# Optimization experiments

Hardware: AMD Instinct MI355X
Metric: run time of the kernel (lower is better)

The kernel has to match this reference:

```python
import jax, jax.numpy as jnp
import numpy as np

TEMPERATURE = 0.1
N, D = 8192, 1024

def setup_inputs() -> dict:
    key = jax.random.key(0)
    k1, k2 = jax.random.split(key)
    im = jax.random.normal(k1, (N, D), dtype=jnp.float32)
    cap = jax.random.normal(k2, (N, D), dtype=jnp.float32)
    return {"im": im, "cap": cap}

def reference(im, cap):
    # InfoNCE (info_nce package) L2-normalizes query, positive and negatives.
    # Per-sample loop: for image i, positive = cap[i], negatives = cap[j != i].
    # Logits set = sim(im_i, cap_j) for all j, positive at j == i, so
    # loss_i = logsumexp_j(S[i, j] / T) - S[i, i] / T  (CLIP-style CE).
    imn = im / jnp.linalg.norm(im, axis=-1, keepdims=True)
    capn = cap / jnp.linalg.norm(cap, axis=-1, keepdims=True)
    S = jnp.einsum('id,jd->ij', imn, capn) / TEMPERATURE  # [N, N]
    diag = jnp.diagonal(S)
    loss_i2c = jax.nn.logsumexp(S, axis=1) - diag  # image -> caption direction
    loss_c2i = jax.nn.logsumexp(S, axis=0) - diag  # caption -> image direction
    # original averages all 2N per-sample losses
    return 0.5 * (jnp.mean(loss_i2c) + jnp.mean(loss_c2i))
```

## Files before the change

kernel.cpp:

```cpp
#include <hip/hip_runtime.h>
#include <stdint.h>

#define N_ 8192
#define D_ 1024
#define EPILOGUE_SCALE (10.0f / 256.0f)
#define ENC_SCALE 16.0f
#define SLAB 262144

typedef float f32x4 __attribute__((ext_vector_type(4)));

#define GLD16(gsrc, ldst)                                                    \
  __builtin_amdgcn_global_load_lds(                                          \
      (const __attribute__((address_space(1))) unsigned int*)(gsrc),         \
      (__attribute__((address_space(3))) unsigned int*)(ldst), 16, 0, 0)


__global__ __launch_bounds__(1024) void normalize_k(
    const float* __restrict__ im, const float* __restrict__ cap,
    unsigned int* __restrict__ imn, unsigned int* __restrict__ capn,
    float* __restrict__ diag, float* __restrict__ sums ) {
  __shared__ unsigned int ldsA[16 * 257];
  __shared__ unsigned int ldsB[16 * 257];
  const int til = blockIdx.x;
  const int t = threadIdx.x;
  if (til < 4) ((float4*)sums)[til * 1024 + t] = (float4){0.f, 0.f, 0.f, 0.f};

  const int r = t >> 6, j = t & 63;
  const int row = til * 16 + r;
  const float4* __restrict__ aR = (const float4*)(im + (size_t)row * D_);
  const float4* __restrict__ bR = (const float4*)(cap + (size_t)row * D_);

  float4 a0 = aR[j], a1 = aR[j + 64], a2 = aR[j + 128], a3 = aR[j + 192];
  float4 b0 = bR[j], b1 = bR[j + 64], b2 = bR[j + 128], b3 = bR[j + 192];

  float ssa = a0.x * a0.x + a0.y * a0.y + a0.z * a0.z + a0.w * a0.w
            + a1.x * a1.x + a1.y * a1.y + a1.z * a1.z + a1.w * a1.w
            + a2.x * a2.x + a2.y * a2.y + a2.z * a2.z + a2.w * a2.w
            + a3.x * a3.x + a3.y * a3.y + a3.z * a3.z + a3.w * a3.w;
  float ssb = b0.x * b0.x + b0.y * b0.y + b0.z * b0.z + b0.w * b0.w
            + b1.x * b1.x + b1.y * b1.y + b1.z * b1.z + b1.w * b1.w
            + b2.x * b2.x + b2.y * b2.y + b2.z * b2.z + b2.w * b2.w
            + b3.x * b3.x + b3.y * b3.y + b3.z * b3.z + b3.w * b3.w;
  float dt  = a0.x * b0.x + a0.y * b0.y + a0.z * b0.z + a0.w * b0.w
            + a1.x * b1.x + a1.y * b1.y + a1.z * b1.z + a1.w * b1.w
            + a2.x * b2.x + a2.y * b2.y + a2.z * b2.z + a2.w * b2.w
            + a3.x * b3.x + a3.y * b3.y + a3.z * b3.z + a3.w * b3.w;
#pragma unroll
  for (int o = 1; o < 64; o <<= 1) {
    ssa += __shfl_xor(ssa, o, 64);
    ssb += __shfl_xor(ssb, o, 64);
    dt  += __shfl_xor(dt, o, 64);
  }
  const float ra = rsqrtf(ssa), rb = rsqrtf(ssb);
  if (j == 0) diag[row] = dt * ra * rb * 10.0f;
  const float sa = ra * ENC_SCALE, sb = rb * ENC_SCALE;

#define CVT_ST(av, bv, ofs)                                                  \
  {                                                                          \
    int pa_ = __builtin_amdgcn_cvt_pk_fp8_f32(av.x * sa, av.y * sa, 0, false); \
    pa_ = __builtin_amdgcn_cvt_pk_fp8_f32(av.z * sa, av.w * sa, pa_, true);  \
    int pb_ = __builtin_amdgcn_cvt_pk_fp8_f32(bv.x * sb, bv.y * sb, 0, false); \
    pb_ = __builtin_amdgcn_cvt_pk_fp8_f32(bv.z * sb, bv.w * sb, pb_, true);  \
    ldsA[r * 257 + j + (ofs)] = (unsigned int)pa_;                           \
    ldsB[r * 257 + j + (ofs)] = (unsigned int)pb_;                           \
  }
  CVT_ST(a0, b0, 0)
  CVT_ST(a1, b1, 64)
  CVT_ST(a2, b2, 128)
  CVT_ST(a3, b3, 192)
#undef CVT_ST
  __syncthreads();

  {
    const int s = t >> 5, c4 = t & 31;
    const int fl0 = c4 * 2, fl1 = fl0 + 1;
    const int i0 = (fl0 & 15) * 257 + s * 8 + (fl0 >> 4) * 2;
    const int i1 = (fl1 & 15) * 257 + s * 8 + (fl1 >> 4) * 2;
    uint4 va, vb;
    va.x = ldsA[i0]; va.y = ldsA[i0 + 1];
    va.z = ldsA[i1]; va.w = ldsA[i1 + 1];
    vb.x = ldsB[i0]; vb.y = ldsB[i0 + 1];
    vb.z = ldsB[i1]; vb.w = ldsB[i1 + 1];
    const size_t d = (size_t)s * 65536 + (size_t)til * 128 + c4 * 4;
    *(uint4*)(imn + d) = va;
    *(uint4*)(capn + d) = vb;
  }
}

__global__ __launch_bounds__(512, 2) void gemm_lse_k(
    const unsigned char* __restrict__ A,
    const unsigned char* __restrict__ B,
    float* __restrict__ rowsum, float* __restrict__ colsum) {
  __shared__ unsigned char lds[4][32768];
  const int t = threadIdx.x;
  const int w = t >> 6, l = t & 63;

  const int bid = blockIdx.x + (blockIdx.y << 5);
  const int nid = (bid & 7) * 128 + (bid >> 3);
  const int rowT = ((nid >> 7) << 2) + (nid & 3);
  const int colT = (nid & 127) >> 2;

  const size_t baseA = (size_t)rowT * 8192;
  const size_t baseB = (size_t)colT * 8192;

  const unsigned char* __restrict__ P = (w < 4) ? A : B;
  const size_t pbase = (w < 4) ? baseA : baseB;
  const int wo = (w & 3) * 4096;
  const int lhalf = (w < 4) ? 0 : 16384;

#define STAGE(kt, cb)                                                        \
  {                                                                          \
    const unsigned char* ps = P + (size_t)(kt) * (2 * (size_t)SLAB) + pbase; \
    _Pragma("unroll")                                                        \
    for (int c = 0; c < 4; ++c) {                                            \
      const int o = wo + c * 1024;                                           \
      GLD16(ps + (size_t)(o >> 13) * SLAB + (o & 8191) + l * 16,             \
            &lds[cb][lhalf + o]);                                            \
    }                                                                        \
  }

  const int wr = w >> 2, wc = w & 3;
  const int aoff = wr * 8 * 512 + l * 8;
  const int boff = 16384 + wc * 4 * 512 + l * 8;

  f32x4 acc[8][4];
#pragma unroll
  for (int m = 0; m < 8; ++m)
#pragma unroll
    for (int n = 0; n < 4; ++n) acc[m][n] = (f32x4){0.f, 0.f, 0.f, 0.f};

#define COMPUTE(cb)                                                          \
  {                                                                          \
    const unsigned char* Lc = &lds[cb][0];                                   \
    _Pragma("unroll")                                                        \
    for (int si = 0; si < 2; ++si) {                                         \
      long a_[8], b_[4];                                                     \
      _Pragma("unroll")                                                      \
      for (int m = 0; m < 8; ++m)                                            \
        a_[m] = *(const long*)(Lc + si * 8192 + aoff + m * 512);             \
      _Pragma("unroll")                                                      \
      for (int n = 0; n < 4; ++n)                                            \
        b_[n] = *(const long*)(Lc + si * 8192 + boff + n * 512);             \
      _Pragma("unroll")                                                      \
      for (int m = 0; m < 8; ++m)                                            \
        _Pragma("unroll")                                                    \
        for (int n = 0; n < 4; ++n)                                          \
          acc[m][n] = __builtin_amdgcn_mfma_f32_16x16x32_fp8_fp8(            \
              a_[m], b_[n], acc[m][n], 0, 0, 0);                             \
    }                                                                        \
  }

  STAGE(0, 0)
  STAGE(1, 1)
  STAGE(2, 2)

#pragma unroll 1
  for (int kt = 0; kt < 13; ++kt) {
    STAGE(kt + 3, (kt + 3) & 3)
    asm volatile("s_waitcnt vmcnt(12)" ::: "memory");
    __builtin_amdgcn_s_barrier();
    COMPUTE(kt & 3)
    __builtin_amdgcn_s_barrier();
  }
  asm volatile("s_waitcnt vmcnt(8)" ::: "memory");
  __builtin_amdgcn_s_barrier();
  COMPUTE(1)
  __builtin_amdgcn_s_barrier();
  asm volatile("s_waitcnt vmcnt(4)" ::: "memory");
  __builtin_amdgcn_s_barrier();
  COMPUTE(2)
  __builtin_amdgcn_s_barrier();
  asm volatile("s_waitcnt vmcnt(0)" ::: "memory");
  __builtin_amdgcn_s_barrier();
  COMPUTE(3)
#undef COMPUTE
#undef STAGE

#pragma unroll
  for (int m = 0; m < 8; ++m)
#pragma unroll
    for (int n = 0; n < 4; ++n)
#pragma unroll
      for (int r = 0; r < 4; ++r)
        acc[m][n][r] = __expf(acc[m][n][r] * EPILOGUE_SCALE);

  const int rowBase = rowT * 256 + wr * 128;
  const int colBase = colT * 256 + wc * 64;
#pragma unroll
  for (int m = 0; m < 8; ++m)
#pragma unroll
    for (int r = 0; r < 4; ++r) {
      float v = 0.f;
#pragma unroll
      for (int n = 0; n < 4; ++n) v += acc[m][n][r];
      v += __shfl_xor(v, 1, 64);
      v += __shfl_xor(v, 2, 64);
      v += __shfl_xor(v, 4, 64);
      v += __shfl_xor(v, 8, 64);
      if ((l & 15) == 0)
        atomicAdd(&rowsum[rowBase + m * 16 + (l >> 4) * 4 + r], v);
    }
#pragma unroll
  for (int n = 0; n < 4; ++n) {
    float v = 0.f;
#pragma unroll
    for (int m = 0; m < 8; ++m)
      v += acc[m][n][0] + acc[m][n][1] + acc[m][n][2] + acc[m][n][3];
    v += __shfl_xor(v, 16, 64);
    v += __shfl_xor(v, 32, 64);
    if (l < 16)
      atomicAdd(&colsum[colBase + n * 16 + l], v);
  }
}

__global__ __launch_bounds__(256) void finalize_k(
    const float* __restrict__ rowsum, const float* __restrict__ colsum,
    const float* __restrict__ diag, float* __restrict__ out) {
  const int t = threadIdx.x;
  float lse = 0.f, dg = 0.f;
  for (int i = t; i < N_; i += 256) {
    lse += __logf(rowsum[i]) + __logf(colsum[i]);
    dg += diag[i];
  }
#pragma unroll
  for (int o = 32; o > 0; o >>= 1) {
    lse += __shfl_down(lse, o, 64);
    dg  += __shfl_down(dg, o, 64);
  }
  __shared__ float red[2][4];
  const int w = t >> 6, l = t & 63;
  if (l == 0) { red[0][w] = lse; red[1][w] = dg; }
  __syncthreads();
  if (t == 0) {
    lse = red[0][0] + red[0][1] + red[0][2] + red[0][3];
    dg  = red[1][0] + red[1][1] + red[1][2] + red[1][3];
    out[0] = 0.5f * lse / (float)N_ - dg / (float)N_;
  }
}

extern "C" void kernel_launch(void* const* d_in, const int* in_sizes, int n_in,
                              void* d_out, int out_size, void* d_ws, size_t ws_size,
                              hipStream_t stream) {
  const float* im = (const float*)d_in[0];
  const float* cap = (const float*)d_in[1];
  float* out = (float*)d_out;
  char* ws = (char*)d_ws;
  unsigned char* imn = (unsigned char*)ws;
  unsigned char* capn = imn + (size_t)N_ * D_;
  float* rowsum = (float*)(ws + 2 * (size_t)N_ * D_);
  float* colsum = rowsum + N_;
  float* diag = colsum + N_;

  normalize_k<<<512, 1024, 0, stream>>>(im, cap, (unsigned int*)imn,
                                        (unsigned int*)capn, diag, rowsum);
  gemm_lse_k<<<dim3(32, 32), 512, 0, stream>>>(imn, capn, rowsum, colsum);
  finalize_k<<<1, 256, 0, stream>>>(rowsum, colsum, diag, out);
}
```

Baseline: 214.7 us.

## Split each k-tile into two phases interleaving LDS reads, global loads and MFMAs

Restructures the FP8 GEMM main loop so each k-tile is processed in two sub-phases. Each phase reads its LDS fragments, issues half of the next tile's global-to-LDS loads, then runs the MFMA block under raised wave priority with a sched_barrier. The aim is finer-grained overlap of memory traffic with matrix math and less contention between waves. The cost is twice as many workgroup barriers per tile, and the hand-placed vmcnt waits must match the new load ordering.

```diff
diff --git a/kernel.cpp b/kernel.cpp
--- a/kernel.cpp
+++ b/kernel.cpp
@@ -108,15 +108,13 @@
   const int wo = (w & 3) * 4096;
   const int lhalf = (w < 4) ? 0 : 16384;
 
-#define STAGE(kt, cb)                                                        \
+#define STAGE2(ps, sb, c0)                                                   \
   {                                                                          \
-    const unsigned char* ps = P + (size_t)(kt) * (2 * (size_t)SLAB) + pbase; \
-    _Pragma("unroll")                                                        \
-    for (int c = 0; c < 4; ++c) {                                            \
-      const int o = wo + c * 1024;                                           \
-      GLD16(ps + (size_t)(o >> 13) * SLAB + (o & 8191) + l * 16,             \
-            &lds[cb][lhalf + o]);                                            \
-    }                                                                        \
+    const int oA_ = wo + (c0) * 1024, oB_ = oA_ + 1024;                      \
+    GLD16((ps) + (size_t)(oA_ >> 13) * SLAB + (oA_ & 8191) + l * 16,         \
+          &lds[sb][lhalf + oA_]);                                            \
+    GLD16((ps) + (size_t)(oB_ >> 13) * SLAB + (oB_ & 8191) + l * 16,         \
+          &lds[sb][lhalf + oB_]);                                            \
   }
 
   const int wr = w >> 2, wc = w & 3;
@@ -129,52 +127,72 @@
 #pragma unroll
     for (int n = 0; n < 4; ++n) acc[m][n] = (f32x4){0.f, 0.f, 0.f, 0.f};
 
-#define COMPUTE(cb)                                                          \
+#define READ_AB(cb, si)                                                      \
+  long a_[8], b_[4];                                                         \
   {                                                                          \
-    const unsigned char* Lc = &lds[cb][0];                                   \
+    const unsigned char* Lc = &lds[cb][(si) * 8192];                         \
     _Pragma("unroll")                                                        \
-    for (int si = 0; si < 2; ++si) {                                         \
-      long a_[8], b_[4];                                                     \
-      _Pragma("unroll")                                                      \
-      for (int m = 0; m < 8; ++m)                                            \
-        a_[m] = *(const long*)(Lc + si * 8192 + aoff + m * 512);             \
-      _Pragma("unroll")                                                      \
-      for (int n = 0; n < 4; ++n)                                            \
-        b_[n] = *(const long*)(Lc + si * 8192 + boff + n * 512);             \
-      _Pragma("unroll")                                                      \
-      for (int m = 0; m < 8; ++m)                                            \
-        _Pragma("unroll")                                                    \
-        for (int n = 0; n < 4; ++n)                                          \
-          acc[m][n] = __builtin_amdgcn_mfma_f32_16x16x32_fp8_fp8(            \
-              a_[m], b_[n], acc[m][n], 0, 0, 0);                             \
-    }                                                                        \
-  }
-
-  STAGE(0, 0)
-  STAGE(1, 1)
-  STAGE(2, 2)
+    for (int m = 0; m < 8; ++m)                                              \
+      a_[m] = *(const long*)(Lc + aoff + m * 512);                           \
+    _Pragma("unroll")                                                        \
+    for (int n = 0; n < 4; ++n)                                              \
+      b_[n] = *(const long*)(Lc + boff + n * 512);                           \
+  }
+
+#define MFMA_ALL                                                             \
+  _Pragma("unroll")                                                          \
+  for (int m = 0; m < 8; ++m)                                                \
+    _Pragma("unroll")                                                        \
+    for (int n = 0; n < 4; ++n)                                              \
+      acc[m][n] = __builtin_amdgcn_mfma_f32_16x16x32_fp8_fp8(                \
+          a_[m], b_[n], acc[m][n], 0, 0, 0);
+
+#define PH_COMPUTE                                                           \
+  __builtin_amdgcn_s_barrier();                                              \
+  asm volatile("s_waitcnt lgkmcnt(0)" ::: "memory");                         \
+  __builtin_amdgcn_sched_barrier(0);                                         \
+  __builtin_amdgcn_s_setprio(1);                                             \
+  MFMA_ALL                                                                   \
+  __builtin_amdgcn_s_setprio(0);                                             \
+  __builtin_amdgcn_s_barrier();
+
+  {
+    const unsigned char* p0 = P + pbase;
+    STAGE2(p0, 0, 0) STAGE2(p0, 0, 2)
+    const unsigned char* p1 = P + 2 * (size_t)SLAB + pbase;
+    STAGE2(p1, 1, 0) STAGE2(p1, 1, 2)
+    const unsigned char* p2 = P + 4 * (size_t)SLAB + pbase;
+    STAGE2(p2, 2, 0) STAGE2(p2, 2, 2)
+  }
+  asm volatile("s_waitcnt vmcnt(8)" ::: "memory");
+  __builtin_amdgcn_s_barrier();
 
 #pragma unroll 1
   for (int kt = 0; kt < 13; ++kt) {
-    STAGE(kt + 3, (kt + 3) & 3)
-    asm volatile("s_waitcnt vmcnt(12)" ::: "memory");
-    __builtin_amdgcn_s_barrier();
-    COMPUTE(kt & 3)
-    __builtin_amdgcn_s_barrier();
-  }
-  asm volatile("s_waitcnt vmcnt(8)" ::: "memory");
-  __builtin_amdgcn_s_barrier();
-  COMPUTE(1)
-  __builtin_amdgcn_s_barrier();
-  asm volatile("s_waitcnt vmcnt(4)" ::: "memory");
-  __builtin_amdgcn_s_barrier();
-  COMPUTE(2)
-  __builtin_amdgcn_s_barrier();
-  asm volatile("s_waitcnt vmcnt(0)" ::: "memory");
-  __builtin_amdgcn_s_barrier();
-  COMPUTE(3)
-#undef COMPUTE
-#undef STAGE
+    const int cb = kt & 3, sb = (kt + 3) & 3;
+    const unsigned char* ps = P + (size_t)(kt + 3) * (2 * (size_t)SLAB) + pbase;
+    {
+      READ_AB(cb, 0)
+      STAGE2(ps, sb, 0)
+      PH_COMPUTE
+    }
+    {
+      READ_AB(cb, 1)
+      STAGE2(ps, sb, 2)
+      asm volatile("s_waitcnt vmcnt(8)" ::: "memory");
+      PH_COMPUTE
+    }
+  }
+  { READ_AB(1, 0) PH_COMPUTE }
+  { READ_AB(1, 1) asm volatile("s_waitcnt vmcnt(4)" ::: "memory"); PH_COMPUTE }
+  { READ_AB(2, 0) PH_COMPUTE }
+  { READ_AB(2, 1) asm volatile("s_waitcnt vmcnt(0)" ::: "memory"); PH_COMPUTE }
+  { READ_AB(3, 0) PH_COMPUTE }
+  { READ_AB(3, 1) PH_COMPUTE }
+#undef PH_COMPUTE
+#undef MFMA_ALL
+#undef READ_AB
+#undef STAGE2
 
 #pragma unroll
   for (int m = 0; m < 8; ++m)
@@ -184,8 +202,8 @@
       for (int r = 0; r < 4; ++r)
         acc[m][n][r] = __expf(acc[m][n][r] * EPILOGUE_SCALE);
 
-  const int rowBase = rowT * 256 + wr * 128;
-  const int colBase = colT * 256 + wc * 64;
+  const int rowBase = rowT * 256 + (w >> 2) * 128;
+  const int colBase = colT * 256 + (w & 3) * 64;
 #pragma unroll
   for (int m = 0; m < 8; ++m)
 #pragma unroll
```

Result: slower. 221.1 us (+3.0%).

## Shrink GEMM tile to 256x128 with double buffering for higher occupancy

Applied to the files above, without the earlier changes.

The fused fp8 GEMM plus exp-sum kernel now uses 256x128 output tiles instead of 256x256, with a 2-stage LDS ring of 24KB buffers instead of a 4-stage ring of 32KB. Block count doubles to 2048 and launch bounds request 4 blocks per CU, with fewer accumulators per wave (4x4 MFMA tiles). The goal is more resident waves to hide latency and better load balance. In exchange, each block reuses operand data less, so L2/global traffic and column atomics go up, and the shallower prefetch pipeline may expose more memory latency.

```diff
diff --git a/kernel.cpp b/kernel.cpp
--- a/kernel.cpp
+++ b/kernel.cpp
@@ -87,62 +87,68 @@
   }
 }
 
-__global__ __launch_bounds__(512, 2) void gemm_lse_k(
+__global__ __launch_bounds__(512, 4) void gemm_lse_k(
     const unsigned char* __restrict__ A,
     const unsigned char* __restrict__ B,
     float* __restrict__ rowsum, float* __restrict__ colsum) {
-  __shared__ unsigned char lds[4][32768];
+  __shared__ unsigned char lds[2][24576];
   const int t = threadIdx.x;
   const int w = t >> 6, l = t & 63;
 
   const int bid = blockIdx.x + (blockIdx.y << 5);
-  const int nid = (bid & 7) * 128 + (bid >> 3);
-  const int rowT = ((nid >> 7) << 2) + (nid & 3);
-  const int colT = (nid & 127) >> 2;
+  const int nid = (bid & 7) * 256 + (bid >> 3);
+  const int rowT = ((nid >> 8) << 2) + (nid & 3);
+  const int colT = (nid >> 2) & 63;
 
   const size_t baseA = (size_t)rowT * 8192;
-  const size_t baseB = (size_t)colT * 8192;
-
-  const unsigned char* __restrict__ P = (w < 4) ? A : B;
-  const size_t pbase = (w < 4) ? baseA : baseB;
-  const int wo = (w & 3) * 4096;
-  const int lhalf = (w < 4) ? 0 : 16384;
-
-#define STAGE(kt, cb)                                                        \
+  const size_t baseB = (size_t)colT * 4096;
+
+  const unsigned char* src[3];
+  int ldsOff[3];
+#pragma unroll
+  for (int c = 0; c < 3; ++c) {
+    const int o = w * 3072 + c * 1024;
+    ldsOff[c] = o;
+    if (o < 16384)
+      src[c] = A + baseA + (size_t)(o >> 13) * SLAB + (o & 8191) + l * 16;
+    else {
+      const int ob = o - 16384;
+      src[c] = B + baseB + (size_t)(ob >> 12) * SLAB + (ob & 4095) + l * 16;
+    }
+  }
+
+#define STAGE(ktv, buf)                                                      \
   {                                                                          \
-    const unsigned char* ps = P + (size_t)(kt) * (2 * (size_t)SLAB) + pbase; \
-    _Pragma("unroll")                                                        \
-    for (int c = 0; c < 4; ++c) {                                            \
-      const int o = wo + c * 1024;                                           \
-      GLD16(ps + (size_t)(o >> 13) * SLAB + (o & 8191) + l * 16,             \
-            &lds[cb][lhalf + o]);                                            \
-    }                                                                        \
-  }
-
-  const int wr = w >> 2, wc = w & 3;
-  const int aoff = wr * 8 * 512 + l * 8;
-  const int boff = 16384 + wc * 4 * 512 + l * 8;
-
-  f32x4 acc[8][4];
-#pragma unroll
-  for (int m = 0; m < 8; ++m)
+    const size_t kofs = (size_t)(ktv) * (2 * (size_t)SLAB);                  \
+    GLD16(src[0] + kofs, &lds[buf][ldsOff[0]]);                              \
+    GLD16(src[1] + kofs, &lds[buf][ldsOff[1]]);                              \
+    GLD16(src[2] + kofs, &lds[buf][ldsOff[2]]);                              \
+  }
+
+  const int wr = w >> 1, wc = w & 1;
+  const int aoff = wr * 2048 + l * 8;
+  const int boff = wc * 2048 + l * 8;
+
+  f32x4 acc[4][4];
+#pragma unroll
+  for (int m = 0; m < 4; ++m)
 #pragma unroll
     for (int n = 0; n < 4; ++n) acc[m][n] = (f32x4){0.f, 0.f, 0.f, 0.f};
 
-#define COMPUTE(cb)                                                          \
+#define COMPUTE(buf)                                                         \
   {                                                                          \
-    const unsigned char* Lc = &lds[cb][0];                                   \
+    const unsigned char* Lc = &lds[buf][0];                                  \
     _Pragma("unroll")                                                        \
     for (int si = 0; si < 2; ++si) {                                         \
-      long a_[8], b_[4];                                                     \
+      long a_[4], b_[4];                                                     \
       _Pragma("unroll")                                                      \
-      for (int m = 0; m < 8; ++m)                                            \
+      for (int m = 0; m < 4; ++m)                                            \
         a_[m] = *(const long*)(Lc + si * 8192 + aoff + m * 512);             \
       _Pragma("unroll")                                                      \
       for (int n = 0; n < 4; ++n)                                            \
-        b_[n] = *(const long*)(Lc + si * 8192 + boff + n * 512);             \
+        b_[n] = *(const long*)(Lc + 16384 + si * 4096 + boff + n * 512);     \
       _Pragma("unroll")                                                      \
-      for (int m = 0; m < 8; ++m)                                            \
+      for (int m = 0; m < 4; ++m)                                            \
         _Pragma("unroll")                                                    \
         for (int n = 0; n < 4; ++n)                                          \
           acc[m][n] = __builtin_amdgcn_mfma_f32_16x16x32_fp8_fp8(            \
@@ -151,43 +157,33 @@
   }
 
   STAGE(0, 0)
-  STAGE(1, 1)
-  STAGE(2, 2)
 
 #pragma unroll 1
-  for (int kt = 0; kt < 13; ++kt) {
-    STAGE(kt + 3, (kt + 3) & 3)
-    asm volatile("s_waitcnt vmcnt(12)" ::: "memory");
+  for (int kt = 0; kt < 15; ++kt) {
+    STAGE(kt + 1, (kt + 1) & 1)
+    asm volatile("s_waitcnt vmcnt(3)" ::: "memory");
     __builtin_amdgcn_s_barrier();
-    COMPUTE(kt & 3)
+    COMPUTE(kt & 1)
     __builtin_amdgcn_s_barrier();
   }
-  asm volatile("s_waitcnt vmcnt(8)" ::: "memory");
+  asm volatile("s_waitcnt vmcnt(0)" ::: "memory");
   __builtin_amdgcn_s_barrier();
   COMPUTE(1)
-  __builtin_amdgcn_s_barrier();
-  asm volatile("s_waitcnt vmcnt(4)" ::: "memory");
-  __builtin_amdgcn_s_barrier();
-  COMPUTE(2)
-  __builtin_amdgcn_s_barrier();
-  asm volatile("s_waitcnt vmcnt(0)" ::: "memory");
-  __builtin_amdgcn_s_barrier();
-  COMPUTE(3)
 #undef COMPUTE
 #undef STAGE
 
 #pragma unroll
-  for (int m = 0; m < 8; ++m)
+  for (int m = 0; m < 4; ++m)
 #pragma unroll
     for (int n = 0; n < 4; ++n)
 #pragma unroll
       for (int r = 0; r < 4; ++r)
         acc[m][n][r] = __expf(acc[m][n][r] * EPILOGUE_SCALE);
 
-  const int rowBase = rowT * 256 + wr * 128;
-  const int colBase = colT * 256 + wc * 64;
-#pragma unroll
-  for (int m = 0; m < 8; ++m)
+  const int rowBase = rowT * 256 + wr * 64;
+  const int colBase = colT * 128 + wc * 64;
+#pragma unroll
+  for (int m = 0; m < 4; ++m)
 #pragma unroll
     for (int r = 0; r < 4; ++r) {
       float v = 0.f;
@@ -204,7 +200,7 @@
   for (int n = 0; n < 4; ++n) {
     float v = 0.f;
 #pragma unroll
-    for (int m = 0; m < 8; ++m)
+    for (int m = 0; m < 4; ++m)
       v += acc[m][n][0] + acc[m][n][1] + acc[m][n][2] + acc[m][n][3];
     v += __shfl_xor(v, 16, 64);
     v += __shfl_xor(v, 32, 64);
@@ -253,6 +249,6 @@
 
   normalize_k<<<512, 1024, 0, stream>>>(im, cap, (unsigned int*)imn,
                                         (unsigned int*)capn, diag, rowsum);
-  gemm_lse_k<<<dim3(32, 32), 512, 0, stream>>>(imn, capn, rowsum, colsum);
+  gemm_lse_k<<<dim3(32, 64), 512, 0, stream>>>(imn, capn, rowsum, colsum);
   finalize_k<<<1, 256, 0, stream>>>(rowsum, colsum, diag, out);
 }
```

Measured after the change: 193.5 us. 1.11x faster.
